# Performance work log

Hardware: AMD Instinct MI355X
Metric: run time of the kernel (lower is better)

Reference implementation:

```python
import jax, jax.numpy as jnp
import numpy as np

B, S, H = 2, 2048, 768
NH, HD = 12, 64
I = 1152
EPS = 1e-5
ROPE_BASE = 10000.0
MAX_POS = 8192


def _layernorm(x, w, b):
    mu = jnp.mean(x, axis=-1, keepdims=True)
    var = jnp.mean(jnp.square(x - mu), axis=-1, keepdims=True)
    return (x - mu) / jnp.sqrt(var + EPS) * w + b


def _rope_tables():
    pos = jnp.arange(MAX_POS, dtype=jnp.float32)
    theta = 1.0 / (ROPE_BASE ** (jnp.arange(0, HD, 2, dtype=jnp.float32) / HD))
    ang = pos[:, None] * theta  # [MAX_POS, HD//2]
    return jnp.cos(ang), jnp.sin(ang)


def _apply_rope(x, cos, sin):
    # x: [B, NH, S, HD]; cos/sin: [B, 1, S, HD//2]; interleaved pair rotation
    x2 = x.reshape(*x.shape[:-1], HD // 2, 2)
    x0, x1 = x2[..., 0], x2[..., 1]
    rot = jnp.stack([x0 * cos - x1 * sin, x1 * cos + x0 * sin], axis=-1)
    return rot.reshape(x.shape)


def setup_inputs() -> dict:
    key = jax.random.key(0)
    ks = jax.random.split(key, 8)
    std = 0.02
    return {
        "hidden_states": jax.random.normal(ks[0], (B, S, H), dtype=jnp.float32),
        "attention_mask": jnp.zeros((B, 1, S, S), dtype=jnp.float32),
        "sliding_window_mask": jnp.zeros((B, 1, S, S), dtype=jnp.float32),
        "position_ids": jnp.tile(jnp.arange(S, dtype=jnp.int32)[None, :], (B, 1)),
        "qkv_w": jax.random.normal(ks[1], (3 * H, H), dtype=jnp.float32) * std,
        "o_w": jax.random.normal(ks[2], (H, H), dtype=jnp.float32) * std,
        "attn_norm_w": jnp.ones((H,), dtype=jnp.float32),
        "attn_norm_b": jnp.zeros((H,), dtype=jnp.float32),
        "mlp_norm_w": jnp.ones((H,), dtype=jnp.float32),
        "mlp_norm_b": jnp.zeros((H,), dtype=jnp.float32),
        "wi_w": jax.random.normal(ks[3], (2 * I, H), dtype=jnp.float32) * std,
        "wi_b": jnp.zeros((2 * I,), dtype=jnp.float32),
        "wo_w": jax.random.normal(ks[4], (H, I), dtype=jnp.float32) * std,
        "wo_b": jnp.zeros((H,), dtype=jnp.float32),
    }


def reference(hidden_states, attention_mask, sliding_window_mask, position_ids,
              qkv_w, o_w, attn_norm_w, attn_norm_b, mlp_norm_w, mlp_norm_b,
              wi_w, wi_b, wo_w, wo_b):
    # --- attention block (layer_id != 0 -> pre-LN) ---
    x = _layernorm(hidden_states, attn_norm_w, attn_norm_b)
    qkv = jnp.einsum('bsh,oh->bso', x, qkv_w)          # [B,S,3H] (no bias)
    qkv = qkv.reshape(B, S, 3, NH, HD)
    qkv = jnp.transpose(qkv, (0, 3, 2, 1, 4))          # [B,NH,3,S,HD]
    q, k, v = qkv[:, :, 0], qkv[:, :, 1], qkv[:, :, 2]

    cos_t, sin_t = _rope_tables()
    cos = cos_t[position_ids][:, None]                 # [B,1,S,HD//2]
    sin = sin_t[position_ids][:, None]
    q = _apply_rope(q, cos, sin)
    k = _apply_rope(k, cos, sin)

    scale = HD ** -0.5
    scores = jnp.einsum('bhqd,bhkd->bhqk', q, k) * scale
    scores = scores + attention_mask + sliding_window_mask
    probs = jax.nn.softmax(scores, axis=-1)
    ctx = jnp.einsum('bhqk,bhkd->bhqd', probs, v)      # [B,NH,S,HD]
    ctx = jnp.transpose(ctx, (0, 2, 1, 3)).reshape(B, S, H)
    attn_out = jnp.einsum('bsh,oh->bso', ctx, o_w)
    hidden = hidden_states + attn_out

    # --- GeGLU MLP block ---
    y = _layernorm(hidden, mlp_norm_w, mlp_norm_b)
    h = jax.nn.gelu(jnp.einsum('bsh,oh->bso', y, wi_w) + wi_b, approximate=False)
    gated = h[..., 0::2] * h[..., 1::2]                # strided gelu-gate split
    mlp_out = jnp.einsum('bsi,oi->bso', gated, wo_w) + wo_b
    return hidden + mlp_out
```

## Files before the change

### kernel.cpp

```cpp
#include <hip/hip_runtime.h>
#include <hip/hip_bf16.h>
#include <math.h>

#define B_  2
#define S_  2048
#define H_  768
#define NH_ 12
#define HD_ 64
#define I_  1152
#define LOG2E 1.4426950408889634f
#define SCALE_L2E 0.18033688011112042f

typedef __bf16 bf16;
typedef __bf16 bf16x8 __attribute__((ext_vector_type(8)));
typedef float  f32x4  __attribute__((ext_vector_type(4)));
typedef float  f32x16 __attribute__((ext_vector_type(16)));
typedef float  f32x2  __attribute__((ext_vector_type(2)));
typedef unsigned u32x2 __attribute__((ext_vector_type(2)));
typedef unsigned u32x4 __attribute__((ext_vector_type(4)));

__device__ __forceinline__ void gll16(const void* g, void* l) {
  __builtin_amdgcn_global_load_lds((const __attribute__((address_space(1))) void*)g,
                                   (__attribute__((address_space(3))) void*)l, 16, 0, 0);
}

__device__ __forceinline__ unsigned pack_bf16(float a, float b) {
  union { bf16 e[2]; unsigned u; } r;
  r.e[0] = (bf16)a; r.e[1] = (bf16)b;
  return r.u;
}

__device__ __forceinline__ void plswap(unsigned &a, unsigned &b) {
  asm volatile("v_permlane32_swap_b32 %0, %1" : "+v"(a), "+v"(b));
}
__device__ __forceinline__ float halfmax(float x) {
  unsigned a = __builtin_bit_cast(unsigned, x), b = a;
  plswap(a, b);
  return fmaxf(__builtin_bit_cast(float, a), __builtin_bit_cast(float, b));
}

#define CN1 442368
#define CN2 147456
#define CN3 442368
#define CN4 221184
__global__ void cvt_all(const float* __restrict__ s0, const float* __restrict__ s1,
                        const float* __restrict__ s2, const float* __restrict__ s3,
                        bf16* __restrict__ d0, bf16* __restrict__ d1,
                        bf16* __restrict__ d2, bf16* __restrict__ d3) {
  int i = blockIdx.x * 256 + threadIdx.x;
  const float* s; bf16* d; int o;
  if (i < CN1)            { s = s0; d = d0; o = i; }
  else if (i < CN1 + CN2) { s = s1; d = d1; o = i - CN1; }
  else if (i < CN1 + CN2 + CN3) { s = s2; d = d2; o = i - CN1 - CN2; }
  else                    { s = s3; d = d3; o = i - CN1 - CN2 - CN3; }
  float4 v = ((const float4*)s)[o];
  union { bf16 e[4]; uint2 u; } r;
  r.e[0] = (bf16)v.x; r.e[1] = (bf16)v.y; r.e[2] = (bf16)v.z; r.e[3] = (bf16)v.w;
  ((uint2*)d)[o] = r.u;
}

__global__ void build_rope_tbl(f32x2* __restrict__ tbl) {
  int i = blockIdx.x * 256 + threadIdx.x;
  int jp = i & 31, pos = i >> 5;
  float th = exp2f((float)jp * (-13.287712379549449f / 32.f));
  float sn, cs;
  sincosf((float)pos * th, &sn, &cs);
  tbl[i] = (f32x2){cs, sn};
}

__global__ __launch_bounds__(256) void combine_mask2(const float* __restrict__ a,
                                                     const float* __restrict__ b,
                                                     bf16* __restrict__ E,
                                                     unsigned* __restrict__ flags) {
  const int kt = blockIdx.x, qi = blockIdx.y, bb = blockIdx.z, tid = threadIdx.x;
  float sm[8][4];
  bool ok = true;
#pragma unroll
  for (int c = 0; c < 8; ++c) {
    int idx4 = c * 256 + tid;
    int r = idx4 >> 4, col = (idx4 & 15) * 4;
    size_t g = ((size_t)(bb * S_) + qi * 128 + r) * S_ + kt * 64 + col;
    float4 x = *(const float4*)(a + g);
    float4 y = *(const float4*)(b + g);
    sm[c][0] = x.x + y.x; sm[c][1] = x.y + y.y;
    sm[c][2] = x.z + y.z; sm[c][3] = x.w + y.w;
    ok = ok && (sm[c][0] == 0.f) && (sm[c][1] == 0.f) && (sm[c][2] == 0.f) && (sm[c][3] == 0.f);
  }
  __shared__ unsigned sh[4];
  unsigned long long bal = __ballot(ok);
  if ((tid & 63) == 0) sh[tid >> 6] = (bal == ~0ull) ? 1u : 0u;
  __syncthreads();
  unsigned flag = sh[0] & sh[1] & sh[2] & sh[3];
  if (tid == 0) flags[(bb * 16 + qi) * 32 + kt] = flag;
  if (!flag) {
#pragma unroll
    for (int c = 0; c < 8; ++c) {
      int idx4 = c * 256 + tid;
      int r = idx4 >> 4, col = (idx4 & 15) * 4;
      size_t g = ((size_t)(bb * S_) + qi * 128 + r) * S_ + kt * 64 + col;
      union { bf16 e[4]; uint2 u; } w;
      w.e[0] = (bf16)__expf(sm[c][0]); w.e[1] = (bf16)__expf(sm[c][1]);
      w.e[2] = (bf16)__expf(sm[c][2]); w.e[3] = (bf16)__expf(sm[c][3]);
      *(uint2*)(E + g) = w.u;
    }
  }
}

__global__ __launch_bounds__(256) void ln_bf16(const float* __restrict__ in,
                                               const float* __restrict__ w,
                                               const float* __restrict__ bia,
                                               bf16* __restrict__ out) {
  int row = blockIdx.x, tid = threadIdx.x;
  const float* x = in + (size_t)row * H_;
  float v0 = x[tid], v1 = x[tid + 256], v2 = x[tid + 512];
  float s = v0 + v1 + v2;
  float q = v0 * v0 + v1 * v1 + v2 * v2;
  for (int o = 1; o < 64; o <<= 1) { s += __shfl_xor(s, o); q += __shfl_xor(q, o); }
  __shared__ float rs[4], rq[4];
  if ((tid & 63) == 0) { rs[tid >> 6] = s; rq[tid >> 6] = q; }
  __syncthreads();
  s = rs[0] + rs[1] + rs[2] + rs[3];
  q = rq[0] + rq[1] + rq[2] + rq[3];
  float mu = s * (1.f / H_);
  float var = q * (1.f / H_) - mu * mu;
  float rstd = rsqrtf(var + 1e-5f);
  bf16* orow = out + (size_t)row * H_;
  orow[tid]       = (bf16)((v0 - mu) * rstd * w[tid]       + bia[tid]);
  orow[tid + 256] = (bf16)((v1 - mu) * rstd * w[tid + 256] + bia[tid + 256]);
  orow[tid + 512] = (bf16)((v2 - mu) * rstd * w[tid + 512] + bia[tid + 512]);
}

__device__ __forceinline__ void gemm_main_loop(
    int K, const bf16* __restrict__ aSrc0, const bf16* __restrict__ aSrc1,
    const bf16* __restrict__ bSrc0, const bf16* __restrict__ bSrc1,
    bf16* As, bf16* Bs, int tid, int wr, int wc, int l15, int lg,
    f32x4 (&acc)[4][4]) {
  const int NT = K >> 5;
  auto stage = [&](int t, int buf) {
    const int ko = t * 32;
    bf16* ad = As + buf * 4096 + tid * 8;
    bf16* bd = Bs + buf * 4096 + tid * 8;
    gll16(aSrc0 + ko, ad);
    gll16(aSrc1 + ko, ad + 2048);
    gll16(bSrc0 + ko, bd);
    gll16(bSrc1 + ko, bd + 2048);
  };
  stage(0, 0);
  __syncthreads();
  for (int t = 0; t < NT; ++t) {
    const int cur = t & 1;
    if (t + 1 < NT) stage(t + 1, cur ^ 1);
    const bf16* Ab = As + cur * 4096;
    const bf16* Bb = Bs + cur * 4096;
    bf16x8 af[4], bfr[4];
#pragma unroll
    for (int i = 0; i < 4; ++i)
      af[i] = *(const bf16x8*)&Ab[(wr + i * 16 + l15) * 32 + lg * 8];
#pragma unroll
    for (int j = 0; j < 4; ++j)
      bfr[j] = *(const bf16x8*)&Bb[(wc + j * 16 + l15) * 32 + lg * 8];
    __builtin_amdgcn_s_setprio(1);
#pragma unroll
    for (int i = 0; i < 4; ++i)
#pragma unroll
      for (int j = 0; j < 4; ++j)
        acc[i][j] = __builtin_amdgcn_mfma_f32_16x16x32_bf16(af[i], bfr[j], acc[i][j], 0, 0, 0);
    __builtin_amdgcn_s_setprio(0);
    __syncthreads();
  }
}

template<bool BIAS, bool RES>
__global__ __launch_bounds__(256) void gemm64d(const bf16* __restrict__ A,
                                               const bf16* __restrict__ W,
                                               float* __restrict__ C,
                                               const float* __restrict__ bias,
                                               const float* __restrict__ res,
                                               int M, int N, int K) {
  __shared__ bf16 As[2 * 64 * 32];
  __shared__ bf16 Bs[2 * 128 * 32];
  const int tid = threadIdx.x, lane = tid & 63, wv = tid >> 6;
  const int bm = blockIdx.y * 64, bn = blockIdx.x * 128;
  const int wr = (wv >> 1) * 32, wc = (wv & 1) * 64;
  const int l15 = lane & 15, lg = lane >> 4;

  f32x4 acc[2][4] = {};
  const int srow = tid >> 2, scc = (tid & 3) * 8;
  const bf16* aSrc0 = A + (size_t)(bm + srow) * K + scc;
  const bf16* bSrc0 = W + (size_t)(bn + srow) * K + scc;
  const bf16* bSrc1 = W + (size_t)(bn + 64 + srow) * K + scc;

  const int NT = K >> 5;
  auto stage = [&](int t, int buf) {
    const int ko = t * 32;
    gll16(aSrc0 + ko, As + buf * 2048 + tid * 8);
    gll16(bSrc0 + ko, Bs + buf * 4096 + tid * 8);
    gll16(bSrc1 + ko, Bs + buf * 4096 + 2048 + tid * 8);
  };
  stage(0, 0);
  __syncthreads();
  for (int t = 0; t < NT; ++t) {
    const int cur = t & 1;
    if (t + 1 < NT) stage(t + 1, cur ^ 1);
    const bf16* Ab = As + cur * 2048;
    const bf16* Bb = Bs + cur * 4096;
    bf16x8 af[2], bfr[4];
#pragma unroll
    for (int i = 0; i < 2; ++i)
      af[i] = *(const bf16x8*)&Ab[(wr + i * 16 + l15) * 32 + lg * 8];
#pragma unroll
    for (int j = 0; j < 4; ++j)
      bfr[j] = *(const bf16x8*)&Bb[(wc + j * 16 + l15) * 32 + lg * 8];
    __builtin_amdgcn_s_setprio(1);
#pragma unroll
    for (int i = 0; i < 2; ++i)
#pragma unroll
      for (int j = 0; j < 4; ++j)
        acc[i][j] = __builtin_amdgcn_mfma_f32_16x16x32_bf16(af[i], bfr[j], acc[i][j], 0, 0, 0);
    __builtin_amdgcn_s_setprio(0);
    __syncthreads();
  }

  const int r0 = lg * 4;
#pragma unroll
  for (int i = 0; i < 2; ++i) {
#pragma unroll
    for (int j = 0; j < 4; ++j) {
      int col = bn + wc + j * 16 + l15;
      float bv = BIAS ? bias[col] : 0.f;
#pragma unroll
      for (int r = 0; r < 4; ++r) {
        int row = bm + wr + i * 16 + r0 + r;
        float v = acc[i][j][r] + bv;
        if (RES) v += res[(size_t)row * N + col];
        C[(size_t)row * N + col] = v;
      }
    }
  }
}

__global__ __launch_bounds__(256) void gemm_qkv(const bf16* __restrict__ A,
                                                const bf16* __restrict__ W,
                                                const int* __restrict__ pid,
                                                const f32x2* __restrict__ tbl,
                                                bf16* __restrict__ qb,
                                                bf16* __restrict__ kb,
                                                bf16* __restrict__ vb) {
  __shared__ bf16 As[2 * 128 * 32];
  __shared__ bf16 Bs[2 * 128 * 32];
  const int tid = threadIdx.x, lane = tid & 63, wv = tid >> 6;
  const int bm = blockIdx.y * 128, bn = blockIdx.x * 128;
  const int wr = (wv >> 1) * 64, wc = (wv & 1) * 64;
  const int l15 = lane & 15, lg = lane >> 4;
  const int K = H_;

  f32x4 acc[4][4] = {};
  const int srow = tid >> 2, scc = (tid & 3) * 8;
  gemm_main_loop(K,
      A + (size_t)(bm + srow) * K + scc, A + (size_t)(bm + 64 + srow) * K + scc,
      W + (size_t)(bn + srow) * K + scc, W + (size_t)(bn + 64 + srow) * K + scc,
      As, Bs, tid, wr, wc, l15, lg, acc);

  const int r0 = lg * 4;
  const int sect = bn / H_;
  const int hcb = (bn % H_) + wc;
  bf16* dst0 = sect == 0 ? qb : (sect == 1 ? kb : vb);
#pragma unroll
  for (int i = 0; i < 4; ++i) {
#pragma unroll
    for (int r = 0; r < 4; ++r) {
      const int row = bm + wr + i * 16 + r0 + r;
      const int b = row >> 11, s = row & 2047;
      const int pos = (sect < 2) ? pid[row] : 0;
#pragma unroll
      for (int j = 0; j < 4; ++j) {
        const int hc = hcb + j * 16 + l15;
        const int h = hc >> 6, d = hc & 63;
        float x = acc[i][j][r];
        float v;
        if (sect < 2) {
          f32x2 cs = tbl[pos * 32 + (d >> 1)];
          float xp = __shfl_xor(x, 1);
          v = (d & 1) ? fmaf(x, cs.x, xp * cs.y) : fmaf(x, cs.x, -xp * cs.y);
        } else {
          v = x;
        }
        dst0[((size_t)(b * NH_ + h) * S_ + s) * HD_ + d] = (bf16)v;
      }
    }
  }
}

__global__ __launch_bounds__(256) void gemm_wi(const bf16* __restrict__ A,
                                               const bf16* __restrict__ W,
                                               const float* __restrict__ bias,
                                               bf16* __restrict__ g) {
  __shared__ bf16 As[2 * 128 * 32];
  __shared__ bf16 Bs[2 * 128 * 32];
  const int tid = threadIdx.x, lane = tid & 63, wv = tid >> 6;
  const int bm = blockIdx.y * 128, bn = blockIdx.x * 128;
  const int wr = (wv >> 1) * 64, wc = (wv & 1) * 64;
  const int l15 = lane & 15, lg = lane >> 4;
  const int K = H_;

  f32x4 acc[4][4] = {};
  const int srow = tid >> 2, scc = (tid & 3) * 8;
  gemm_main_loop(K,
      A + (size_t)(bm + srow) * K + scc, A + (size_t)(bm + 64 + srow) * K + scc,
      W + (size_t)(bn + srow) * K + scc, W + (size_t)(bn + 64 + srow) * K + scc,
      As, Bs, tid, wr, wc, l15, lg, acc);

  const int r0 = lg * 4;
#pragma unroll
  for (int j = 0; j < 4; ++j) {
    const int col = bn + wc + j * 16 + l15;
    const float bv = bias[col];
#pragma unroll
    for (int i = 0; i < 4; ++i) {
#pragma unroll
      for (int r = 0; r < 4; ++r) {
        const int row = bm + wr + i * 16 + r0 + r;
        float x = acc[i][j][r] + bv;
        float gx = 0.5f * x * (1.f + erff(x * 0.70710678118654752f));
        float gp = __shfl_xor(gx, 1);
        if (!(l15 & 1))
          g[(size_t)row * I_ + (col >> 1)] = (bf16)(gx * gp);
      }
    }
  }
}

__global__ __launch_bounds__(256, 3) void attn4L(
    const bf16* __restrict__ Q, const bf16* __restrict__ Kg, const bf16* __restrict__ Vg,
    const bf16* __restrict__ Eg, const unsigned* __restrict__ flags, bf16* __restrict__ ctx) {
  __shared__ bf16 Ks[2][64 * 64];
  __shared__ bf16 Vt[2][2][64 * 64];
  const int tid = threadIdx.x, lane = tid & 63, wv = tid >> 6;
  const int wq = wv & 1, ks = wv >> 1;
  const int qi = blockIdx.x, h = blockIdx.y, b = blockIdx.z;
  const int l31 = lane & 31, hi = lane >> 5, b4 = (lane >> 4) & 1;
  const size_t headbase = (size_t)(b * NH_ + h) * S_ * HD_;
  const bf16* kbase = Kg + headbase;
  const bf16* vbase = Vg + headbase;
  const unsigned* fptr = flags + (b * 16 + (qi >> 1)) * 32;
  const int kswz = (l31 & 7) << 4;
  const int qrow = qi * 64 + wq * 32 + l31;
  const bf16* Erow = Eg + (size_t)b * S_ * S_ + (size_t)qrow * S_;

  union { unsigned u[4]; bf16x8 v; } ones;
  ones.u[0] = ones.u[1] = ones.u[2] = ones.u[3] = 0x3F803F80u;

  bf16x8 qf[4];
  {
    const bf16* qp = Q + headbase + (size_t)qrow * HD_;
#pragma unroll
    for (int kc = 0; kc < 4; ++kc)
      qf[kc] = *(const bf16x8*)(qp + kc * 16 + hi * 8);
  }

  auto stageK = [&](int t, int par) {
#pragma unroll
    for (int c = 0; c < 2; ++c) {
      int ch = c * 256 + tid, kr = ch >> 3, sl = ch & 7;
      gll16(kbase + (size_t)t * 64 * HD_ + kr * HD_ + (sl ^ (kr & 7)) * 8, &Ks[par][ch * 8]);
    }
  };
  auto stageV = [&](int t, int bs, int par) {
#pragma unroll
    for (int c = 0; c < 2; ++c) {
      int ch = c * 256 + tid;
      int p = ch >> 7, kr = (ch & 127) >> 1, hf = ch & 1;
      gll16(vbase + (size_t)t * 64 * HD_ + kr * HD_ + (p >> 1) * 32 + (p & 1) * 16 + hf * 8,
            &Vt[bs][par][ch * 8]);
    }
  };

  float m = -1e30f, l = 0.f;
  f32x16 oa[2] = {};

  stageK(0, 0); stageK(1, 1);
  stageV(0, 0, 0); stageV(1, 0, 1);
  unsigned fl = fptr[ks];
  __syncthreads();

  for (int R = 0; R < 16; ++R) {
    const int cur = R & 1;
    const int kt = 2 * R + ks;

    f32x16 sv[2];
    __builtin_amdgcn_s_setprio(1);
#pragma unroll
    for (int kb = 0; kb < 2; ++kb) {
      f32x16 s = {};
#pragma unroll
      for (int kc = 0; kc < 4; ++kc) {
        const bf16x8 kf = *(const bf16x8*)((const char*)&Ks[ks][0] +
            ((kb * 32 + l31) * 128 + ((kc * 32 + hi * 16) ^ kswz)));
        s = __builtin_amdgcn_mfma_f32_32x32x16_bf16(kf, qf[kc], s, 0, 0, 0);
      }
      sv[kb] = s;
    }
    __builtin_amdgcn_s_setprio(0);

    __syncthreads();

    unsigned flN = 1;
    if (R < 15) {
      flN = fptr[kt + 2];
      stageK(2 * R + 2, 0); stageK(2 * R + 3, 1);
      stageV(2 * R + 2, cur ^ 1, 0); stageV(2 * R + 3, cur ^ 1, 1);
    }

    float p0 = fmaxf(sv[0][0], sv[1][0]), p1 = fmaxf(sv[0][1], sv[1][1]);
    float p2 = fmaxf(sv[0][2], sv[1][2]), p3 = fmaxf(sv[0][3], sv[1][3]);
#pragma unroll
    for (int r2 = 4; r2 < 16; r2 += 4) {
      p0 = fmaxf(p0, fmaxf(sv[0][r2],     sv[1][r2]));
      p1 = fmaxf(p1, fmaxf(sv[0][r2 + 1], sv[1][r2 + 1]));
      p2 = fmaxf(p2, fmaxf(sv[0][r2 + 2], sv[1][r2 + 2]));
      p3 = fmaxf(p3, fmaxf(sv[0][r2 + 3], sv[1][r2 + 3]));
    }
    float pmS = halfmax(fmaxf(fmaxf(p0, p1), fmaxf(p2, p3))) * SCALE_L2E;
    if (__any(pmS - m > 8.f)) {
      float mn = fmaxf(m, pmS);
      float alpha = exp2f(m - mn);
      m = mn;
      l *= alpha;
#pragma unroll
      for (int db = 0; db < 2; ++db)
#pragma unroll
        for (int r2 = 0; r2 < 16; ++r2) oa[db][r2] *= alpha;
    }
#pragma unroll
    for (int kb = 0; kb < 2; ++kb)
#pragma unroll
      for (int r2 = 0; r2 < 16; ++r2)
        sv[kb][r2] = exp2f(fmaf(sv[kb][r2], SCALE_L2E, -m));
    if (!fl) {
#pragma unroll
      for (int kb = 0; kb < 2; ++kb)
#pragma unroll
        for (int rq = 0; rq < 4; ++rq) {
          union { bf16 e[4]; u32x2 u; } eu;
          eu.u = *(const u32x2*)(Erow + (size_t)kt * 64 + kb * 32 + rq * 8 + hi * 4);
#pragma unroll
          for (int j = 0; j < 4; ++j)
            sv[kb][rq * 4 + j] *= (float)eu.e[j];
        }
    }

    unsigned pk[2][4][2];
#pragma unroll
    for (int kb = 0; kb < 2; ++kb)
#pragma unroll
      for (int rq = 0; rq < 4; ++rq)
#pragma unroll
        for (int dd = 0; dd < 2; ++dd)
          pk[kb][rq][dd] = pack_bf16(sv[kb][rq * 4 + dd * 2], sv[kb][rq * 4 + dd * 2 + 1]);
    union { u32x4 u; bf16x8 v; } pauv[4];
#pragma unroll
    for (int kc = 0; kc < 4; ++kc) {
      const int kb = kc >> 1, rb = (kc & 1) * 2;
      unsigned pa0[2], pa1[2];
#pragma unroll
      for (int dd = 0; dd < 2; ++dd) {
        unsigned A = pk[kb][rb][dd], Bv = pk[kb][rb + 1][dd];
        plswap(A, Bv);
        pa0[dd] = A; pa1[dd] = Bv;
      }
      pauv[kc].u = (u32x4){pa0[0], pa0[1], pa1[0], pa1[1]};
    }

    {
      f32x16 ls = {};
#pragma unroll
      for (int kc = 0; kc < 4; ++kc)
        ls = __builtin_amdgcn_mfma_f32_32x32x16_bf16(ones.v, pauv[kc].v, ls, 0, 0, 0);
      l += ls[0];
    }

    const unsigned vlds = (unsigned)(size_t)&Vt[cur][ks][0] + b4 * 1920;
#pragma unroll
    for (int db = 0; db < 2; ++db) {
      u32x2 tr[4][2];
#pragma unroll
      for (int kc = 0; kc < 4; ++kc)
#pragma unroll
        for (int rd = 0; rd < 2; ++rd) {
          unsigned ad = vlds + (db * 4096 + kc * 512 + rd * 128);
          asm volatile("ds_read_b64_tr_b16 %0, %1 offset:0" : "=v"(tr[kc][rd]) : "v"(ad));
        }
      asm volatile("s_waitcnt lgkmcnt(0)" ::: "memory");
      __builtin_amdgcn_sched_barrier(0);
      __builtin_amdgcn_s_setprio(1);
#pragma unroll
      for (int kc = 0; kc < 4; ++kc) {
        union { u32x4 u; bf16x8 v; } vfu;
        vfu.u = (u32x4){tr[kc][0][0], tr[kc][0][1], tr[kc][1][0], tr[kc][1][1]};
        oa[db] = __builtin_amdgcn_mfma_f32_32x32x16_bf16(vfu.v, pauv[kc].v, oa[db], 0, 0, 0);
      }
      __builtin_amdgcn_s_setprio(0);
    }
    __syncthreads();
    fl = flN;
  }

  float* KO = (float*)&Ks[0][0];
  float* ML = (float*)&Vt[1][0][0];
  char*  TR = (char*)&Vt[1][0][0] + 512;
  if (ks == 1) {
#pragma unroll
    for (int db = 0; db < 2; ++db)
#pragma unroll
      for (int rq = 0; rq < 4; ++rq) {
        int q4 = (db * 4 + rq) ^ (l31 & 7);
        *(f32x4*)&KO[wq * 2048 + l31 * 64 + hi * 32 + q4 * 4] =
            (f32x4){oa[db][rq * 4], oa[db][rq * 4 + 1], oa[db][rq * 4 + 2], oa[db][rq * 4 + 3]};
      }
    if (hi == 0) { ML[wq * 64 + l31 * 2] = m; ML[wq * 64 + l31 * 2 + 1] = l; }
  }
  __syncthreads();
  if (ks == 0) {
    float m1 = ML[wq * 64 + l31 * 2], l1 = ML[wq * 64 + l31 * 2 + 1];
    float ms = fmaxf(m, m1);
    float a0 = exp2f(m - ms), a1 = exp2f(m1 - ms);
    float inv = 1.f / (l * a0 + l1 * a1);
    a0 *= inv; a1 *= inv;
#pragma unroll
    for (int db = 0; db < 2; ++db)
#pragma unroll
      for (int rq = 0; rq < 4; ++rq) {
        int q4 = (db * 4 + rq) ^ (l31 & 7);
        f32x4 o1 = *(const f32x4*)&KO[wq * 2048 + l31 * 64 + hi * 32 + q4 * 4];
        float f0 = oa[db][rq * 4 + 0] * a0 + o1[0] * a1;
        float f1 = oa[db][rq * 4 + 1] * a0 + o1[1] * a1;
        float f2 = oa[db][rq * 4 + 2] * a0 + o1[2] * a1;
        float f3 = oa[db][rq * 4 + 3] * a0 + o1[3] * a1;
        u32x2 w = (u32x2){pack_bf16(f0, f1), pack_bf16(f2, f3)};
        *(u32x2*)(TR + wq * 4096 + l31 * 128 + ((db * 64 + rq * 16 + hi * 8) ^ kswz)) = w;
      }
  }
  __syncthreads();
#pragma unroll
  for (int c = 0; c < 2; ++c) {
    int ch = c * 256 + tid, q = ch >> 3, sl = ch & 7;
    u32x4 vv = *(const u32x4*)(TR + ((q >> 5) * 4096 + (q & 31) * 128 + ((sl ^ (q & 7)) * 16)));
    *(u32x4*)(ctx + ((size_t)(b * S_) + qi * 64 + q) * H_ + h * HD_ + sl * 8) = vv;
  }
}

extern "C" void kernel_launch(void* const* d_in, const int* in_sizes, int n_in,
                              void* d_out, int out_size, void* d_ws, size_t ws_size,
                              hipStream_t stream) {
  const float* hs   = (const float*)d_in[0];
  const float* am   = (const float*)d_in[1];
  const float* swm  = (const float*)d_in[2];
  const int*   pid  = (const int*)d_in[3];
  const float* qkvw = (const float*)d_in[4];
  const float* ow   = (const float*)d_in[5];
  const float* anw  = (const float*)d_in[6];
  const float* anb  = (const float*)d_in[7];
  const float* mnw  = (const float*)d_in[8];
  const float* mnb  = (const float*)d_in[9];
  const float* wiw  = (const float*)d_in[10];
  const float* wib  = (const float*)d_in[11];
  const float* wow  = (const float*)d_in[12];
  const float* wob  = (const float*)d_in[13];
  float* out = (float*)d_out;

  char* ws = (char*)d_ws;
  size_t off = 0;
  auto alloc = [&](size_t bytes) { void* p = ws + off; off += (bytes + 255) & ~255ull; return p; };

  bf16* wqkv_b = (bf16*)alloc((size_t)3 * H_ * H_ * 2);
  bf16* wo_b   = (bf16*)alloc((size_t)H_ * H_ * 2);
  bf16* wwi_b  = (bf16*)alloc((size_t)2 * I_ * H_ * 2);
  bf16* wwo_b  = (bf16*)alloc((size_t)H_ * I_ * 2);
  bf16* xln    = (bf16*)alloc((size_t)B_ * S_ * H_ * 2);
  bf16* qb     = (bf16*)alloc((size_t)B_ * NH_ * S_ * HD_ * 2);
  bf16* kb     = (bf16*)alloc((size_t)B_ * NH_ * S_ * HD_ * 2);
  bf16* vb     = (bf16*)alloc((size_t)B_ * NH_ * S_ * HD_ * 2);
  bf16* Eg     = (bf16*)alloc((size_t)B_ * S_ * S_ * 2);
  unsigned* flg= (unsigned*)alloc((size_t)B_ * 16 * 32 * 4);
  bf16* ctx    = (bf16*)alloc((size_t)B_ * S_ * H_ * 2);
  float* hid2  = (float*)alloc((size_t)B_ * S_ * H_ * 4);
  bf16* gated  = (bf16*)alloc((size_t)B_ * S_ * I_ * 2);
  f32x2* tbl   = (f32x2*)alloc((size_t)8192 * 32 * 8);
  (void)ws_size; (void)n_in; (void)in_sizes; (void)out_size;

  const int rows = B_ * S_;

  cvt_all<<<(CN1 + CN2 + CN3 + CN4) / 256, 256, 0, stream>>>(
      qkvw, ow, wiw, wow, wqkv_b, wo_b, wwi_b, wwo_b);
  build_rope_tbl<<<8192 * 32 / 256, 256, 0, stream>>>(tbl);
  combine_mask2<<<dim3(32, 16, B_), 256, 0, stream>>>(am, swm, Eg, flg);

  ln_bf16<<<rows, 256, 0, stream>>>(hs, anw, anb, xln);
  gemm_qkv<<<dim3(3 * H_ / 128, rows / 128), 256, 0, stream>>>(
      xln, wqkv_b, pid, tbl, qb, kb, vb);
  attn4L<<<dim3(S_ / 64, NH_, B_), 256, 0, stream>>>(qb, kb, vb, Eg, flg, ctx);
  gemm64d<false, true><<<dim3(H_ / 128, rows / 64), 256, 0, stream>>>(
      ctx, wo_b, hid2, nullptr, hs, rows, H_, H_);
  ln_bf16<<<rows, 256, 0, stream>>>(hid2, mnw, mnb, xln);
  gemm_wi<<<dim3(2 * I_ / 128, rows / 128), 256, 0, stream>>>(xln, wwi_b, wib, gated);
  gemm64d<true, true><<<dim3(H_ / 128, rows / 64), 256, 0, stream>>>(
      gated, wwo_b, out, wob, hid2, rows, H_, I_);
}
```

Measured before the change: 205.2 us.

## Merge prep kernels and co-schedule mask combine with QKV GEMM

Weight conversion, RoPE table construction and the first LayerNorm are folded into one launch that picks its role from the block index. The mask-combine work is moved into the QKV GEMM launch as extra blocks, reusing the GEMM shared buffer for the ballot flags. This cuts four launches and their gaps, and lets the memory-bound mask pass overlap the compute-bound GEMM. The merged kernels may use more registers, which can lower occupancy, and the block order may schedule the work unevenly.

```diff
diff --git a/kernel.cpp b/kernel.cpp
--- a/kernel.cpp
+++ b/kernel.cpp
@@ -43,66 +43,56 @@
 #define CN2 147456
 #define CN3 442368
 #define CN4 221184
-__global__ void cvt_all(const float* __restrict__ s0, const float* __restrict__ s1,
-                        const float* __restrict__ s2, const float* __restrict__ s3,
-                        bf16* __restrict__ d0, bf16* __restrict__ d1,
-                        bf16* __restrict__ d2, bf16* __restrict__ d3) {
-  int i = blockIdx.x * 256 + threadIdx.x;
-  const float* s; bf16* d; int o;
-  if (i < CN1)            { s = s0; d = d0; o = i; }
-  else if (i < CN1 + CN2) { s = s1; d = d1; o = i - CN1; }
-  else if (i < CN1 + CN2 + CN3) { s = s2; d = d2; o = i - CN1 - CN2; }
-  else                    { s = s3; d = d3; o = i - CN1 - CN2 - CN3; }
-  float4 v = ((const float4*)s)[o];
-  union { bf16 e[4]; uint2 u; } r;
-  r.e[0] = (bf16)v.x; r.e[1] = (bf16)v.y; r.e[2] = (bf16)v.z; r.e[3] = (bf16)v.w;
-  ((uint2*)d)[o] = r.u;
-}
-
-__global__ void build_rope_tbl(f32x2* __restrict__ tbl) {
-  int i = blockIdx.x * 256 + threadIdx.x;
-  int jp = i & 31, pos = i >> 5;
-  float th = exp2f((float)jp * (-13.287712379549449f / 32.f));
-  float sn, cs;
-  sincosf((float)pos * th, &sn, &cs);
-  tbl[i] = (f32x2){cs, sn};
-}
-
-__global__ __launch_bounds__(256) void combine_mask2(const float* __restrict__ a,
-                                                     const float* __restrict__ b,
-                                                     bf16* __restrict__ E,
-                                                     unsigned* __restrict__ flags) {
-  const int kt = blockIdx.x, qi = blockIdx.y, bb = blockIdx.z, tid = threadIdx.x;
-  float sm[8][4];
-  bool ok = true;
-#pragma unroll
-  for (int c = 0; c < 8; ++c) {
-    int idx4 = c * 256 + tid;
-    int r = idx4 >> 4, col = (idx4 & 15) * 4;
-    size_t g = ((size_t)(bb * S_) + qi * 128 + r) * S_ + kt * 64 + col;
-    float4 x = *(const float4*)(a + g);
-    float4 y = *(const float4*)(b + g);
-    sm[c][0] = x.x + y.x; sm[c][1] = x.y + y.y;
-    sm[c][2] = x.z + y.z; sm[c][3] = x.w + y.w;
-    ok = ok && (sm[c][0] == 0.f) && (sm[c][1] == 0.f) && (sm[c][2] == 0.f) && (sm[c][3] == 0.f);
-  }
-  __shared__ unsigned sh[4];
-  unsigned long long bal = __ballot(ok);
-  if ((tid & 63) == 0) sh[tid >> 6] = (bal == ~0ull) ? 1u : 0u;
-  __syncthreads();
-  unsigned flag = sh[0] & sh[1] & sh[2] & sh[3];
-  if (tid == 0) flags[(bb * 16 + qi) * 32 + kt] = flag;
-  if (!flag) {
-#pragma unroll
-    for (int c = 0; c < 8; ++c) {
-      int idx4 = c * 256 + tid;
-      int r = idx4 >> 4, col = (idx4 & 15) * 4;
-      size_t g = ((size_t)(bb * S_) + qi * 128 + r) * S_ + kt * 64 + col;
-      union { bf16 e[4]; uint2 u; } w;
-      w.e[0] = (bf16)__expf(sm[c][0]); w.e[1] = (bf16)__expf(sm[c][1]);
-      w.e[2] = (bf16)__expf(sm[c][2]); w.e[3] = (bf16)__expf(sm[c][3]);
-      *(uint2*)(E + g) = w.u;
-    }
+#define CVT_BLKS  ((CN1 + CN2 + CN3 + CN4) / 256)
+#define ROPE_BLKS 1024
+#define LN_BLKS   4096
+
+__global__ __launch_bounds__(256) void prep(
+    const float* __restrict__ qkvw, const float* __restrict__ ow,
+    const float* __restrict__ wiw,  const float* __restrict__ wow,
+    bf16* __restrict__ wqkv_b, bf16* __restrict__ wo_b,
+    bf16* __restrict__ wwi_b,  bf16* __restrict__ wwo_b,
+    f32x2* __restrict__ tbl,
+    const float* __restrict__ hs, const float* __restrict__ anw,
+    const float* __restrict__ anb, bf16* __restrict__ xln) {
+  __shared__ float rs[4], rq[4];
+  const int blk = blockIdx.x, tid = threadIdx.x;
+  if (blk < CVT_BLKS) {
+    int i = blk * 256 + tid;
+    const float* s; bf16* d; int o;
+    if (i < CN1)                  { s = qkvw; d = wqkv_b; o = i; }
+    else if (i < CN1 + CN2)       { s = ow;   d = wo_b;   o = i - CN1; }
+    else if (i < CN1 + CN2 + CN3) { s = wiw;  d = wwi_b;  o = i - CN1 - CN2; }
+    else                          { s = wow;  d = wwo_b;  o = i - CN1 - CN2 - CN3; }
+    float4 v = ((const float4*)s)[o];
+    union { bf16 e[4]; uint2 u; } r;
+    r.e[0] = (bf16)v.x; r.e[1] = (bf16)v.y; r.e[2] = (bf16)v.z; r.e[3] = (bf16)v.w;
+    ((uint2*)d)[o] = r.u;
+  } else if (blk < CVT_BLKS + ROPE_BLKS) {
+    int i = (blk - CVT_BLKS) * 256 + tid;
+    int jp = i & 31, pos = i >> 5;
+    float th = exp2f((float)jp * (-13.287712379549449f / 32.f));
+    float sn, cs;
+    sincosf((float)pos * th, &sn, &cs);
+    tbl[i] = (f32x2){cs, sn};
+  } else {
+    int row = blk - CVT_BLKS - ROPE_BLKS;
+    const float* x = hs + (size_t)row * H_;
+    float v0 = x[tid], v1 = x[tid + 256], v2 = x[tid + 512];
+    float s = v0 + v1 + v2;
+    float q = v0 * v0 + v1 * v1 + v2 * v2;
+    for (int o = 1; o < 64; o <<= 1) { s += __shfl_xor(s, o); q += __shfl_xor(q, o); }
+    if ((tid & 63) == 0) { rs[tid >> 6] = s; rq[tid >> 6] = q; }
+    __syncthreads();
+    s = rs[0] + rs[1] + rs[2] + rs[3];
+    q = rq[0] + rq[1] + rq[2] + rq[3];
+    float mu = s * (1.f / H_);
+    float var = q * (1.f / H_) - mu * mu;
+    float rstd = rsqrtf(var + 1e-5f);
+    bf16* orow = xln + (size_t)row * H_;
+    orow[tid]       = (bf16)((v0 - mu) * rstd * anw[tid]       + anb[tid]);
+    orow[tid + 256] = (bf16)((v1 - mu) * rstd * anw[tid + 256] + anb[tid + 256]);
+    orow[tid + 512] = (bf16)((v2 - mu) * rstd * anw[tid + 512] + anb[tid + 512]);
   }
 }
 
@@ -239,53 +229,90 @@
   }
 }
 
-__global__ __launch_bounds__(256) void gemm_qkv(const bf16* __restrict__ A,
-                                                const bf16* __restrict__ W,
-                                                const int* __restrict__ pid,
-                                                const f32x2* __restrict__ tbl,
-                                                bf16* __restrict__ qb,
-                                                bf16* __restrict__ kb,
-                                                bf16* __restrict__ vb) {
+__global__ __launch_bounds__(256) void gemm_qkv_mask(
+    const bf16* __restrict__ A, const bf16* __restrict__ W,
+    const int* __restrict__ pid, const f32x2* __restrict__ tbl,
+    bf16* __restrict__ qb, bf16* __restrict__ kb, bf16* __restrict__ vb,
+    const float* __restrict__ am, const float* __restrict__ swm,
+    bf16* __restrict__ E, unsigned* __restrict__ flags) {
   __shared__ bf16 As[2 * 128 * 32];
   __shared__ bf16 Bs[2 * 128 * 32];
-  const int tid = threadIdx.x, lane = tid & 63, wv = tid >> 6;
-  const int bm = blockIdx.y * 128, bn = blockIdx.x * 128;
-  const int wr = (wv >> 1) * 64, wc = (wv & 1) * 64;
-  const int l15 = lane & 15, lg = lane >> 4;
-  const int K = H_;
-
-  f32x4 acc[4][4] = {};
-  const int srow = tid >> 2, scc = (tid & 3) * 8;
-  gemm_main_loop(K,
-      A + (size_t)(bm + srow) * K + scc, A + (size_t)(bm + 64 + srow) * K + scc,
-      W + (size_t)(bn + srow) * K + scc, W + (size_t)(bn + 64 + srow) * K + scc,
-      As, Bs, tid, wr, wc, l15, lg, acc);
-
-  const int r0 = lg * 4;
-  const int sect = bn / H_;
-  const int hcb = (bn % H_) + wc;
-  bf16* dst0 = sect == 0 ? qb : (sect == 1 ? kb : vb);
-#pragma unroll
-  for (int i = 0; i < 4; ++i) {
-#pragma unroll
-    for (int r = 0; r < 4; ++r) {
-      const int row = bm + wr + i * 16 + r0 + r;
-      const int b = row >> 11, s = row & 2047;
-      const int pos = (sect < 2) ? pid[row] : 0;
-#pragma unroll
-      for (int j = 0; j < 4; ++j) {
-        const int hc = hcb + j * 16 + l15;
-        const int h = hc >> 6, d = hc & 63;
-        float x = acc[i][j][r];
-        float v;
-        if (sect < 2) {
-          f32x2 cs = tbl[pos * 32 + (d >> 1)];
-          float xp = __shfl_xor(x, 1);
-          v = (d & 1) ? fmaf(x, cs.x, xp * cs.y) : fmaf(x, cs.x, -xp * cs.y);
-        } else {
-          v = x;
+  const int blk = blockIdx.x, tid = threadIdx.x;
+
+  if (blk < 576) {
+    const int lane = tid & 63, wv = tid >> 6;
+    const int bm = (blk / 18) * 128, bn = (blk % 18) * 128;
+    const int wr = (wv >> 1) * 64, wc = (wv & 1) * 64;
+    const int l15 = lane & 15, lg = lane >> 4;
+    const int K = H_;
+
+    f32x4 acc[4][4] = {};
+    const int srow = tid >> 2, scc = (tid & 3) * 8;
+    gemm_main_loop(K,
+        A + (size_t)(bm + srow) * K + scc, A + (size_t)(bm + 64 + srow) * K + scc,
+        W + (size_t)(bn + srow) * K + scc, W + (size_t)(bn + 64 + srow) * K + scc,
+        As, Bs, tid, wr, wc, l15, lg, acc);
+
+    const int r0 = lg * 4;
+    const int sect = bn / H_;
+    const int hcb = (bn % H_) + wc;
+    bf16* dst0 = sect == 0 ? qb : (sect == 1 ? kb : vb);
+#pragma unroll
+    for (int i = 0; i < 4; ++i) {
+#pragma unroll
+      for (int r = 0; r < 4; ++r) {
+        const int row = bm + wr + i * 16 + r0 + r;
+        const int b = row >> 11, s = row & 2047;
+        const int pos = (sect < 2) ? pid[row] : 0;
+#pragma unroll
+        for (int j = 0; j < 4; ++j) {
+          const int hc = hcb + j * 16 + l15;
+          const int h = hc >> 6, d = hc & 63;
+          float x = acc[i][j][r];
+          float v;
+          if (sect < 2) {
+            f32x2 cs = tbl[pos * 32 + (d >> 1)];
+            float xp = __shfl_xor(x, 1);
+            v = (d & 1) ? fmaf(x, cs.x, xp * cs.y) : fmaf(x, cs.x, -xp * cs.y);
+          } else {
+            v = x;
+          }
+          dst0[((size_t)(b * NH_ + h) * S_ + s) * HD_ + d] = (bf16)v;
         }
-        dst0[((size_t)(b * NH_ + h) * S_ + s) * HD_ + d] = (bf16)v;
+      }
+    }
+  } else {
+    const int mb = blk - 576;
+    const int kt = mb & 31, qi = (mb >> 5) & 15, bb = mb >> 9;
+    float sm[8][4];
+    bool ok = true;
+#pragma unroll
+    for (int c = 0; c < 8; ++c) {
+      int idx4 = c * 256 + tid;
+      int r = idx4 >> 4, col = (idx4 & 15) * 4;
+      size_t g = ((size_t)(bb * S_) + qi * 128 + r) * S_ + kt * 64 + col;
+      float4 x = *(const float4*)(am + g);
+      float4 y = *(const float4*)(swm + g);
+      sm[c][0] = x.x + y.x; sm[c][1] = x.y + y.y;
+      sm[c][2] = x.z + y.z; sm[c][3] = x.w + y.w;
+      ok = ok && (sm[c][0] == 0.f) && (sm[c][1] == 0.f) && (sm[c][2] == 0.f) && (sm[c][3] == 0.f);
+    }
+    unsigned* sh = (unsigned*)As;
+    unsigned long long bal = __ballot(ok);
+    if ((tid & 63) == 0) sh[tid >> 6] = (bal == ~0ull) ? 1u : 0u;
+    __syncthreads();
+    unsigned flag = sh[0] & sh[1] & sh[2] & sh[3];
+    if (tid == 0) flags[(bb * 16 + qi) * 32 + kt] = flag;
+    if (!flag) {
+#pragma unroll
+      for (int c = 0; c < 8; ++c) {
+        int idx4 = c * 256 + tid;
+        int r = idx4 >> 4, col = (idx4 & 15) * 4;
+        size_t g = ((size_t)(bb * S_) + qi * 128 + r) * S_ + kt * 64 + col;
+        union { bf16 e[4]; uint2 u; } w;
+        w.e[0] = (bf16)__expf(sm[c][0]); w.e[1] = (bf16)__expf(sm[c][1]);
+        w.e[2] = (bf16)__expf(sm[c][2]); w.e[3] = (bf16)__expf(sm[c][3]);
+        *(uint2*)(E + g) = w.u;
       }
     }
   }
@@ -590,14 +617,10 @@
 
   const int rows = B_ * S_;
 
-  cvt_all<<<(CN1 + CN2 + CN3 + CN4) / 256, 256, 0, stream>>>(
-      qkvw, ow, wiw, wow, wqkv_b, wo_b, wwi_b, wwo_b);
-  build_rope_tbl<<<8192 * 32 / 256, 256, 0, stream>>>(tbl);
-  combine_mask2<<<dim3(32, 16, B_), 256, 0, stream>>>(am, swm, Eg, flg);
-
-  ln_bf16<<<rows, 256, 0, stream>>>(hs, anw, anb, xln);
-  gemm_qkv<<<dim3(3 * H_ / 128, rows / 128), 256, 0, stream>>>(
-      xln, wqkv_b, pid, tbl, qb, kb, vb);
+  prep<<<CVT_BLKS + ROPE_BLKS + LN_BLKS, 256, 0, stream>>>(
+      qkvw, ow, wiw, wow, wqkv_b, wo_b, wwi_b, wwo_b, tbl, hs, anw, anb, xln);
+  gemm_qkv_mask<<<576 + 1024, 256, 0, stream>>>(
+      xln, wqkv_b, pid, tbl, qb, kb, vb, am, swm, Eg, flg);
   attn4L<<<dim3(S_ / 64, NH_, B_), 256, 0, stream>>>(qb, kb, vb, Eg, flg, ctx);
   gemm64d<false, true><<<dim3(H_ / 128, rows / 64), 256, 0, stream>>>(
       ctx, wo_b, hid2, nullptr, hs, rows, H_, H_);
```

After: 216.0 us. +5.2%, slower.
